# Kernel tuning notes

Measured on AMD Instinct MI355X. Metric: run time of the kernel, lower is better.

The kernel has to match this reference:

```python
import jax, jax.numpy as jnp
import numpy as np

B, S, E, H = 4, 2048, 1024, 16
D = E // H  # head dim = 64

def setup_inputs() -> dict:
    key = jax.random.key(0)
    k1, k2, k3 = jax.random.split(key, 3)
    scale = 0.02
    return {
        "x": jax.random.normal(k1, (B, S, E), dtype=jnp.float32),
        "W_qkv": jax.random.normal(k2, (E, 3 * E), dtype=jnp.float32) * scale,
        "b_qkv": jnp.zeros((3 * E,), dtype=jnp.float32),
        "W_o": jax.random.normal(k3, (E, E), dtype=jnp.float32) * scale,
        "b_o": jnp.zeros((E,), dtype=jnp.float32),
    }

def reference(x, W_qkv, b_qkv, W_o, b_o):
    # dropout is identity in eval mode
    qkv = x @ W_qkv + b_qkv                      # [B, S, 3E]
    q, k, v = jnp.split(qkv, 3, axis=-1)          # each [B, S, E]
    def split_heads(t):
        return t.reshape(B, S, H, D).transpose(0, 2, 1, 3)  # [B, H, S, D]
    q, k, v = split_heads(q), split_heads(k), split_heads(v)
    scores = jnp.einsum("bhsd,bhtd->bhst", q, k) / jnp.sqrt(jnp.float32(D))
    causal = jnp.tril(jnp.ones((S, S), dtype=bool))
    scores = jnp.where(causal[None, None], scores, jnp.float32(-jnp.inf))
    attn = jax.nn.softmax(scores, axis=-1)        # [B, H, S, S]
    out = jnp.einsum("bhst,bhtd->bhsd", attn, v)  # [B, H, S, D]
    out = out.transpose(0, 2, 1, 3).reshape(B, S, E)
    return out @ W_o + b_o
```

## Files before the change

### kernel.cpp

```cpp
#include <hip/hip_runtime.h>
#include <stdint.h>

typedef __bf16 bf16_t;
typedef __bf16 bf16x8 __attribute__((ext_vector_type(8)));
typedef float f32x4 __attribute__((ext_vector_type(4)));

#define LOG2E 1.44269504088896340736f

__device__ __forceinline__ float fexp2(float x) {
#if __has_builtin(__builtin_amdgcn_exp2f)
    return __builtin_amdgcn_exp2f(x);
#else
    return exp2f(x);
#endif
}

__device__ __forceinline__ void gld_lds16(const bf16_t* g, bf16_t* l) {
    __builtin_amdgcn_global_load_lds(
        (__attribute__((address_space(1))) void*)(bf16_t*)g,
        (__attribute__((address_space(3))) void*)l,
        16, 0, 0);
}

__global__ __launch_bounds__(256) void prep_k(
    const float* __restrict__ x, bf16_t* __restrict__ xb,
    const float* __restrict__ Wqkv, bf16_t* __restrict__ wqkvT,
    const float* __restrict__ Wo, bf16_t* __restrict__ woT)
{
    __shared__ float t[32][33];
    const int tid = threadIdx.x;
    int blk = blockIdx.x;
    if (blk < 8192) {
        int i = blk * 1024 + tid * 4;
        float4 v = *(const float4*)(x + i);
        union { bf16_t b[4]; uint2 u; } u;
        u.b[0] = (bf16_t)v.x; u.b[1] = (bf16_t)v.y; u.b[2] = (bf16_t)v.z; u.b[3] = (bf16_t)v.w;
        *(uint2*)(xb + i) = u.u;
        return;
    }
    const float* in; bf16_t* out; int C, bx, by;
    if (blk < 11264) { blk -= 8192; in = Wqkv; out = wqkvT; C = 3072; bx = blk % 96; by = blk / 96; }
    else             { blk -= 11264; in = Wo;   out = woT;   C = 1024; bx = blk % 32; by = blk / 32; }
    const int R = 1024;
    const int tx = tid & 31, ty = tid >> 5;
    const int c0 = bx * 32, r0 = by * 32;
    #pragma unroll
    for (int j = 0; j < 32; j += 8)
        t[ty + j][tx] = in[(size_t)(r0 + ty + j) * C + c0 + tx];
    __syncthreads();
    #pragma unroll
    for (int j = 0; j < 32; j += 8)
        out[(size_t)(c0 + ty + j) * R + r0 + tx] = (bf16_t)t[tx][ty + j];
}

__device__ __forceinline__ void gemm128_body(
    const bf16_t* __restrict__ A, const bf16_t* __restrict__ Bt,
    bf16_t* Al, bf16_t* Bl, f32x4 (&acc)[4][4], int m0, int n0, int Kd)
{
    const int tid = threadIdx.x;
    const int w = tid >> 6, lane = tid & 63;
    const int l15 = lane & 15, quad = lane >> 4;
    const int wm = w >> 1, wn = w & 1;

    const int srow = lane >> 3;
    const int scg = ((lane & 7) ^ srow) * 8;
    const bf16_t* Ag = A + (size_t)(m0 + w * 32 + srow) * Kd + scg;
    const bf16_t* Bg = Bt + (size_t)(n0 + w * 32 + srow) * Kd + scg;
    bf16_t* Ald = Al + (w * 32) * 64;
    bf16_t* Bld = Bl + (w * 32) * 64;

    const int rc0 = (quad ^ (l15 & 7)) * 8;
    const int rc1 = ((quad + 4) ^ (l15 & 7)) * 8;

    for (int k0 = 0; k0 < Kd; k0 += 64) {
        __syncthreads();
        #pragma unroll
        for (int j = 0; j < 4; j++) {
            gld_lds16(Ag + k0 + (size_t)(j * 8) * Kd, Ald + (j * 8) * 64);
            gld_lds16(Bg + k0 + (size_t)(j * 8) * Kd, Bld + (j * 8) * 64);
        }
        __syncthreads();

        #pragma unroll
        for (int hh = 0; hh < 2; hh++) {
            const int rc = hh ? rc1 : rc0;
            bf16x8 af[4], bf[4];
            #pragma unroll
            for (int mi = 0; mi < 4; mi++)
                af[mi] = *(const bf16x8*)(Al + (wm * 64 + mi * 16 + l15) * 64 + rc);
            #pragma unroll
            for (int ni = 0; ni < 4; ni++)
                bf[ni] = *(const bf16x8*)(Bl + (wn * 64 + ni * 16 + l15) * 64 + rc);
            #pragma unroll
            for (int mi = 0; mi < 4; mi++)
                #pragma unroll
                for (int ni = 0; ni < 4; ni++)
                    acc[mi][ni] = __builtin_amdgcn_mfma_f32_16x16x32_bf16(
                        af[mi], bf[ni], acc[mi][ni], 0, 0, 0);
        }
    }
}

__global__ __launch_bounds__(256) void gemm_qkv_k(
    const bf16_t* __restrict__ X, const bf16_t* __restrict__ WT,
    const float* __restrict__ bias,
    bf16_t* __restrict__ Qb, bf16_t* __restrict__ Kb, bf16_t* __restrict__ VTb)
{
    __shared__ bf16_t Al[128 * 64];
    __shared__ bf16_t Bl[128 * 64];
    const int tid = threadIdx.x;
    const int lane = tid & 63, w = tid >> 6;
    const int l15 = lane & 15, quad = lane >> 4;
    const int wm = w >> 1, wn = w & 1;
    const int n0 = blockIdx.x * 128;
    const int m0 = blockIdx.y * 128;

    f32x4 acc[4][4];
    #pragma unroll
    for (int mi = 0; mi < 4; mi++)
        #pragma unroll
        for (int ni = 0; ni < 4; ni++) acc[mi][ni] = (f32x4){0.f, 0.f, 0.f, 0.f};

    gemm128_body(WT, X, Al, Bl, acc, m0, n0, 1024);

    const float QSCALE = 0.125f * LOG2E;
    const int region = m0 >> 10;
    #pragma unroll
    for (int mi = 0; mi < 4; mi++) {
        const int mbase = m0 + wm * 64 + mi * 16 + quad * 4;
        const float4 bia = *(const float4*)(bias + mbase);
        const float ba[4] = {bia.x, bia.y, bia.z, bia.w};
        const int col = mbase & 1023;
        const int h = col >> 6, dbase = col & 63;
        #pragma unroll
        for (int ni = 0; ni < 4; ni++) {
            const int n = n0 + wn * 64 + ni * 16 + l15;
            const int b = n >> 11, s = n & 2047;
            if (region == 0) {
                union { bf16_t bv[4]; uint2 u; } u;
                #pragma unroll
                for (int r = 0; r < 4; r++)
                    u.bv[r] = (bf16_t)((acc[mi][ni][r] + ba[r]) * QSCALE);
                *(uint2*)(Qb + (((size_t)b * 16 + h) * 2048 + s) * 64 + dbase) = u.u;
            } else if (region == 1) {
                union { bf16_t bv[4]; uint2 u; } u;
                #pragma unroll
                for (int r = 0; r < 4; r++)
                    u.bv[r] = (bf16_t)(acc[mi][ni][r] + ba[r]);
                *(uint2*)(Kb + (((size_t)b * 16 + h) * 2048 + s) * 64 + dbase) = u.u;
            } else {
                bf16_t* dst = VTb + (((size_t)b * 16 + h) * 64 + dbase) * 2048 + s;
                #pragma unroll
                for (int r = 0; r < 4; r++)
                    dst[(size_t)r * 2048] = (bf16_t)(acc[mi][ni][r] + ba[r]);
            }
        }
    }
}

__global__ __launch_bounds__(256) void attn_k(
    const bf16_t* __restrict__ Qb, const bf16_t* __restrict__ Kb,
    const bf16_t* __restrict__ VTb, bf16_t* __restrict__ Ob)
{
    __shared__ bf16_t Kl[64 * 64];
    __shared__ bf16_t Vl[64 * 64];
    __shared__ bf16_t Pl[4][16 * 72];

    const int tid = threadIdx.x;
    const int w = tid >> 6, lane = tid & 63;
    const int l15 = lane & 15, quad = lane >> 4;
    const int idx = blockIdx.x;
    const int qt = 31 - (idx >> 6);
    const int bh = idx & 63;
    const int b = bh >> 4, h = bh & 15;
    const int q0 = qt * 64;

    const bf16_t* Qp = Qb + (size_t)bh * 2048 * 64;
    const bf16_t* Kp = Kb + (size_t)bh * 2048 * 64;
    const bf16_t* Vp = VTb + (size_t)bh * 64 * 2048;

    const int srow = w * 16 + (lane >> 3);
    const int scol = ((lane & 7) ^ ((lane >> 3) & 7)) * 8;
    const int rc0 = (quad ^ (l15 & 7)) * 8;
    const int rc1 = ((quad + 4) ^ (l15 & 7)) * 8;

    const int qrow = q0 + w * 16 + l15;
    bf16x8 aq0 = *(const bf16x8*)(Qp + (size_t)qrow * 64 + quad * 8);
    bf16x8 aq1 = *(const bf16x8*)(Qp + (size_t)qrow * 64 + 32 + quad * 8);

    bf16x8 vone;
    #pragma unroll
    for (int j = 0; j < 8; j++) vone[j] = (bf16_t)1.0f;

    f32x4 o[4];
    #pragma unroll
    for (int ni = 0; ni < 4; ni++) o[ni] = (f32x4){0.f, 0.f, 0.f, 0.f};
    f32x4 lacc = (f32x4){0.f, 0.f, 0.f, 0.f};
    const int qloc = w * 16 + l15;

    for (int kv0 = 0; kv0 <= q0; kv0 += 64) {
        __syncthreads();
        gld_lds16(Kp + (size_t)(kv0 + srow) * 64 + scol, Kl + (w * 16) * 64);
        gld_lds16(Kp + (size_t)(kv0 + srow + 8) * 64 + scol, Kl + (w * 16 + 8) * 64);
        gld_lds16(Vp + (size_t)srow * 2048 + kv0 + scol, Vl + (w * 16) * 64);
        gld_lds16(Vp + (size_t)(srow + 8) * 2048 + kv0 + scol, Vl + (w * 16 + 8) * 64);
        __syncthreads();

        f32x4 sv[4];
        #pragma unroll
        for (int ni = 0; ni < 4; ni++) {
            bf16x8 ak0 = *(const bf16x8*)(Kl + (ni * 16 + l15) * 64 + rc0);
            bf16x8 ak1 = *(const bf16x8*)(Kl + (ni * 16 + l15) * 64 + rc1);
            f32x4 z = (f32x4){0.f, 0.f, 0.f, 0.f};
            z = __builtin_amdgcn_mfma_f32_16x16x32_bf16(ak0, aq0, z, 0, 0, 0);
            z = __builtin_amdgcn_mfma_f32_16x16x32_bf16(ak1, aq1, z, 0, 0, 0);
            sv[ni] = z;
        }

        if (kv0 == q0) {
            #pragma unroll
            for (int ni = 0; ni < 4; ni++)
                #pragma unroll
                for (int r = 0; r < 4; r++)
                    if (ni * 16 + quad * 4 + r > qloc) sv[ni][r] = -INFINITY;
        }

        #pragma unroll
        for (int ni = 0; ni < 4; ni++) {
            union { bf16_t bv[4]; uint2 u; } pk;
            #pragma unroll
            for (int r = 0; r < 4; r++) pk.bv[r] = (bf16_t)fexp2(sv[ni][r]);
            *(uint2*)(&Pl[w][l15 * 72 + ni * 16 + quad * 4]) = pk.u;
        }

        bf16x8 pa0 = *(const bf16x8*)(&Pl[w][l15 * 72 + quad * 8]);
        bf16x8 pa1 = *(const bf16x8*)(&Pl[w][l15 * 72 + 32 + quad * 8]);
        #pragma unroll
        for (int ni = 0; ni < 4; ni++) {
            bf16x8 bv0 = *(const bf16x8*)(Vl + (ni * 16 + l15) * 64 + rc0);
            bf16x8 bv1 = *(const bf16x8*)(Vl + (ni * 16 + l15) * 64 + rc1);
            o[ni] = __builtin_amdgcn_mfma_f32_16x16x32_bf16(bv0, pa0, o[ni], 0, 0, 0);
            o[ni] = __builtin_amdgcn_mfma_f32_16x16x32_bf16(bv1, pa1, o[ni], 0, 0, 0);
        }
        lacc = __builtin_amdgcn_mfma_f32_16x16x32_bf16(vone, pa0, lacc, 0, 0, 0);
        lacc = __builtin_amdgcn_mfma_f32_16x16x32_bf16(vone, pa1, lacc, 0, 0, 0);
    }

    const float inv = 1.0f / lacc[0];
    const int s = q0 + w * 16 + l15;
    bf16_t* obase = Ob + ((size_t)b * 2048 + s) * 1024 + h * 64;
    #pragma unroll
    for (int ni = 0; ni < 4; ni++) {
        union { bf16_t bv[4]; uint2 u; } u;
        #pragma unroll
        for (int r = 0; r < 4; r++) u.bv[r] = (bf16_t)(o[ni][r] * inv);
        *(uint2*)(obase + ni * 16 + quad * 4) = u.u;
    }
}

__global__ __launch_bounds__(256) void gemm_out_k(
    const bf16_t* __restrict__ O, const bf16_t* __restrict__ WT,
    const float* __restrict__ bias, float* __restrict__ out)
{
    __shared__ bf16_t Al[128 * 64];
    __shared__ bf16_t Bl[128 * 64];
    const int tid = threadIdx.x;
    const int lane = tid & 63, w = tid >> 6;
    const int l15 = lane & 15, quad = lane >> 4;
    const int wm = w >> 1, wn = w & 1;
    const int n0 = blockIdx.x * 128;
    const int m0 = blockIdx.y * 128;

    f32x4 acc[4][4];
    #pragma unroll
    for (int mi = 0; mi < 4; mi++)
        #pragma unroll
        for (int ni = 0; ni < 4; ni++) acc[mi][ni] = (f32x4){0.f, 0.f, 0.f, 0.f};

    gemm128_body(WT, O, Al, Bl, acc, m0, n0, 1024);

    #pragma unroll
    for (int mi = 0; mi < 4; mi++) {
        const int mbase = m0 + wm * 64 + mi * 16 + quad * 4;
        const float4 bia = *(const float4*)(bias + mbase);
        #pragma unroll
        for (int ni = 0; ni < 4; ni++) {
            const int n = n0 + wn * 64 + ni * 16 + l15;
            float4 v;
            v.x = acc[mi][ni][0] + bia.x;
            v.y = acc[mi][ni][1] + bia.y;
            v.z = acc[mi][ni][2] + bia.z;
            v.w = acc[mi][ni][3] + bia.w;
            *(float4*)(out + (size_t)n * 1024 + mbase) = v;
        }
    }
}


extern "C" void kernel_launch(void* const* d_in, const int* in_sizes, int n_in,
                              void* d_out, int out_size, void* d_ws, size_t ws_size,
                              hipStream_t stream) {
    const float* x     = (const float*)d_in[0];
    const float* W_qkv = (const float*)d_in[1];
    const float* b_qkv = (const float*)d_in[2];
    const float* W_o   = (const float*)d_in[3];
    const float* b_o   = (const float*)d_in[4];
    float* out = (float*)d_out;

    char* ws = (char*)d_ws;
    size_t off = 0;
    auto alloc = [&](size_t bytes) -> void* {
        void* p = ws + off;
        off += (bytes + 255) & ~(size_t)255;
        return p;
    };
    bf16_t* xb    = (bf16_t*)alloc((size_t)8192 * 1024 * 2);
    bf16_t* wqkvT = (bf16_t*)alloc((size_t)3072 * 1024 * 2);
    bf16_t* woT   = (bf16_t*)alloc((size_t)1024 * 1024 * 2);
    bf16_t* Qb    = (bf16_t*)alloc((size_t)8192 * 1024 * 2);
    bf16_t* Kb    = (bf16_t*)alloc((size_t)8192 * 1024 * 2);
    bf16_t* VTb   = (bf16_t*)alloc((size_t)8192 * 1024 * 2);
    bf16_t* Ob    = xb;

    prep_k<<<12288, 256, 0, stream>>>(x, xb, W_qkv, wqkvT, W_o, woT);
    gemm_qkv_k<<<dim3(64, 24), 256, 0, stream>>>(xb, wqkvT, b_qkv, Qb, Kb, VTb);
    attn_k<<<2048, 256, 0, stream>>>(Qb, Kb, VTb, Ob);
    gemm_out_k<<<dim3(64, 8), 256, 0, stream>>>(Ob, woT, b_o, out);
}
```

Before: 247.3 us.

## Use 256x128 tiles with 3-stage LDS pipeline in projection GEMMs

Replaces the single-buffered GEMM main loop with a three-stage global-to-LDS pipeline that issues loads two K-steps ahead and waits with vmcnt counters instead of two full barriers per step. Blocks grow to 512 threads covering 256x128 output tiles, so the B operand is shared across more rows. MFMA sections are raised in priority with s_setprio. This adds LDS use (about 144KB per block), which limits occupancy, and the grids halve, so fewer blocks are available to fill the CUs.

```diff
diff --git a/kernel.cpp b/kernel.cpp
--- a/kernel.cpp
+++ b/kernel.cpp
@@ -53,9 +53,9 @@
         out[(size_t)(c0 + ty + j) * R + r0 + tx] = (bf16_t)t[tx][ty + j];
 }
 
-__device__ __forceinline__ void gemm128_body(
+__device__ __forceinline__ void gemm_body_3deep(
     const bf16_t* __restrict__ A, const bf16_t* __restrict__ Bt,
-    bf16_t* Al, bf16_t* Bl, f32x4 (&acc)[4][4], int m0, int n0, int Kd)
+    bf16_t* Al, bf16_t* Bl, f32x4 (&acc)[4][4], int m0, int n0)
 {
     const int tid = threadIdx.x;
     const int w = tid >> 6, lane = tid & 63;
@@ -64,56 +64,78 @@
 
     const int srow = lane >> 3;
     const int scg = ((lane & 7) ^ srow) * 8;
-    const bf16_t* Ag = A + (size_t)(m0 + w * 32 + srow) * Kd + scg;
-    const bf16_t* Bg = Bt + (size_t)(n0 + w * 32 + srow) * Kd + scg;
+    const bf16_t* Ag = A  + (size_t)(m0 + w * 32 + srow) * 1024 + scg;
+    const bf16_t* Bg = Bt + (size_t)(n0 + w * 16 + srow) * 1024 + scg;
     bf16_t* Ald = Al + (w * 32) * 64;
-    bf16_t* Bld = Bl + (w * 32) * 64;
+    bf16_t* Bld = Bl + (w * 16) * 64;
 
     const int rc0 = (quad ^ (l15 & 7)) * 8;
     const int rc1 = ((quad + 4) ^ (l15 & 7)) * 8;
 
-    for (int k0 = 0; k0 < Kd; k0 += 64) {
-        __syncthreads();
-        #pragma unroll
-        for (int j = 0; j < 4; j++) {
-            gld_lds16(Ag + k0 + (size_t)(j * 8) * Kd, Ald + (j * 8) * 64);
-            gld_lds16(Bg + k0 + (size_t)(j * 8) * Kd, Bld + (j * 8) * 64);
-        }
-        __syncthreads();
-
+    auto stage = [&](int t, int s) {
+        const int koff = t * 64;
+        #pragma unroll
+        for (int j = 0; j < 4; j++)
+            gld_lds16(Ag + koff + (size_t)(j * 8) * 1024,
+                      Ald + s * 16384 + (j * 8) * 64);
+        #pragma unroll
+        for (int j = 0; j < 2; j++)
+            gld_lds16(Bg + koff + (size_t)(j * 8) * 1024,
+                      Bld + s * 8192 + (j * 8) * 64);
+    };
+
+    stage(0, 0);
+    stage(1, 1);
+    asm volatile("s_waitcnt vmcnt(6)" ::: "memory");
+    __builtin_amdgcn_s_barrier();
+
+    int cur = 0, stg = 2;
+    for (int t = 0; t < 16; ++t) {
+        if (t < 14) stage(t + 2, stg);
+        const bf16_t* Ab = Al + cur * 16384;
+        const bf16_t* Bb = Bl + cur * 8192;
         #pragma unroll
         for (int hh = 0; hh < 2; hh++) {
             const int rc = hh ? rc1 : rc0;
-            bf16x8 af[4], bf[4];
+            bf16x8 af[4], bfr[4];
             #pragma unroll
             for (int mi = 0; mi < 4; mi++)
-                af[mi] = *(const bf16x8*)(Al + (wm * 64 + mi * 16 + l15) * 64 + rc);
+                af[mi] = *(const bf16x8*)(Ab + (wm * 64 + mi * 16 + l15) * 64 + rc);
             #pragma unroll
             for (int ni = 0; ni < 4; ni++)
-                bf[ni] = *(const bf16x8*)(Bl + (wn * 64 + ni * 16 + l15) * 64 + rc);
+                bfr[ni] = *(const bf16x8*)(Bb + (wn * 64 + ni * 16 + l15) * 64 + rc);
+            __builtin_amdgcn_s_setprio(1);
             #pragma unroll
             for (int mi = 0; mi < 4; mi++)
                 #pragma unroll
                 for (int ni = 0; ni < 4; ni++)
                     acc[mi][ni] = __builtin_amdgcn_mfma_f32_16x16x32_bf16(
-                        af[mi], bf[ni], acc[mi][ni], 0, 0, 0);
-        }
-    }
-}
-
-__global__ __launch_bounds__(256) void gemm_qkv_k(
+                        af[mi], bfr[ni], acc[mi][ni], 0, 0, 0);
+            __builtin_amdgcn_s_setprio(0);
+        }
+        if (t < 15) {
+            if (t < 14) asm volatile("s_waitcnt vmcnt(6)" ::: "memory");
+            else        asm volatile("s_waitcnt vmcnt(0)" ::: "memory");
+            __builtin_amdgcn_s_barrier();
+        }
+        cur = (cur == 2) ? 0 : cur + 1;
+        stg = (stg == 2) ? 0 : stg + 1;
+    }
+}
+
+__global__ __launch_bounds__(512) void gemm_qkv_k(
     const bf16_t* __restrict__ X, const bf16_t* __restrict__ WT,
     const float* __restrict__ bias,
     bf16_t* __restrict__ Qb, bf16_t* __restrict__ Kb, bf16_t* __restrict__ VTb)
 {
-    __shared__ bf16_t Al[128 * 64];
-    __shared__ bf16_t Bl[128 * 64];
+    __shared__ bf16_t Al[3 * 256 * 64];
+    __shared__ bf16_t Bl[3 * 128 * 64];
     const int tid = threadIdx.x;
     const int lane = tid & 63, w = tid >> 6;
     const int l15 = lane & 15, quad = lane >> 4;
     const int wm = w >> 1, wn = w & 1;
     const int n0 = blockIdx.x * 128;
-    const int m0 = blockIdx.y * 128;
+    const int m0 = blockIdx.y * 256;
 
     f32x4 acc[4][4];
     #pragma unroll
@@ -121,7 +143,7 @@
         #pragma unroll
         for (int ni = 0; ni < 4; ni++) acc[mi][ni] = (f32x4){0.f, 0.f, 0.f, 0.f};
 
-    gemm128_body(WT, X, Al, Bl, acc, m0, n0, 1024);
+    gemm_body_3deep(WT, X, Al, Bl, acc, m0, n0);
 
     const float QSCALE = 0.125f * LOG2E;
     const int region = m0 >> 10;
@@ -258,18 +280,18 @@
     }
 }
 
-__global__ __launch_bounds__(256) void gemm_out_k(
+__global__ __launch_bounds__(512) void gemm_out_k(
     const bf16_t* __restrict__ O, const bf16_t* __restrict__ WT,
     const float* __restrict__ bias, float* __restrict__ out)
 {
-    __shared__ bf16_t Al[128 * 64];
-    __shared__ bf16_t Bl[128 * 64];
+    __shared__ bf16_t Al[3 * 256 * 64];
+    __shared__ bf16_t Bl[3 * 128 * 64];
     const int tid = threadIdx.x;
     const int lane = tid & 63, w = tid >> 6;
     const int l15 = lane & 15, quad = lane >> 4;
     const int wm = w >> 1, wn = w & 1;
     const int n0 = blockIdx.x * 128;
-    const int m0 = blockIdx.y * 128;
+    const int m0 = blockIdx.y * 256;
 
     f32x4 acc[4][4];
     #pragma unroll
@@ -277,7 +299,7 @@
         #pragma unroll
         for (int ni = 0; ni < 4; ni++) acc[mi][ni] = (f32x4){0.f, 0.f, 0.f, 0.f};
 
-    gemm128_body(WT, O, Al, Bl, acc, m0, n0, 1024);
+    gemm_body_3deep(WT, O, Al, Bl, acc, m0, n0);
 
     #pragma unroll
     for (int mi = 0; mi < 4; mi++) {
@@ -323,7 +345,7 @@
     bf16_t* Ob    = xb;
 
     prep_k<<<12288, 256, 0, stream>>>(x, xb, W_qkv, wqkvT, W_o, woT);
-    gemm_qkv_k<<<dim3(64, 24), 256, 0, stream>>>(xb, wqkvT, b_qkv, Qb, Kb, VTb);
+    gemm_qkv_k<<<dim3(64, 12), 512, 0, stream>>>(xb, wqkvT, b_qkv, Qb, Kb, VTb);
     attn_k<<<2048, 256, 0, stream>>>(Qb, Kb, VTb, Ob);
-    gemm_out_k<<<dim3(64, 8), 256, 0, stream>>>(Ob, woT, b_o, out);
-}
+    gemm_out_k<<<dim3(64, 4), 512, 0, stream>>>(Ob, woT, b_o, out);
+}
```

Result: slower. 255.3 us (+3.2%).
